# Kernel optimization log

Measured on AMD Instinct MI355X. Metric: run time of the kernel, lower is better.

## Reference

```python
import jax, jax.numpy as jnp
import numpy as np

B, S, D, H = 4, 2048, 1024, 16
DK = D // H
THETA = 10000.0


def apply_rope(x, pos, theta):
    # x: [B, H, S, DK], pos: [S] int
    d = x.shape[-1]
    inv_freq = theta ** (-jnp.arange(0, d, 2, dtype=jnp.float32) / d)  # [d/2]
    ang = pos.astype(jnp.float32)[:, None] * inv_freq[None, :]          # [S, d/2]
    cos, sin = jnp.cos(ang), jnp.sin(ang)
    x1 = x[..., 0::2]
    x2 = x[..., 1::2]
    r1 = x1 * cos - x2 * sin
    r2 = x1 * sin + x2 * cos
    return jnp.stack([r1, r2], axis=-1).reshape(x.shape)


def setup_inputs() -> dict:
    key = jax.random.key(0)
    ks = jax.random.split(key, 5)
    scale = 1.0 / np.sqrt(D)
    x = jax.random.normal(ks[0], (B, S, D), dtype=jnp.float32)
    Wq = jax.random.normal(ks[1], (D, D), dtype=jnp.float32) * scale
    Wk = jax.random.normal(ks[2], (D, D), dtype=jnp.float32) * scale
    Wv = jax.random.normal(ks[3], (D, D), dtype=jnp.float32) * scale
    Wo = jax.random.normal(ks[4], (D, D), dtype=jnp.float32) * scale
    token_positions = jnp.arange(S, dtype=jnp.int32)
    return {"x": x, "token_positions": token_positions,
            "Wq": Wq, "Wk": Wk, "Wv": Wv, "Wo": Wo}


def reference(x, token_positions, Wq, Wk, Wv, Wo):
    b, s, d = x.shape
    # Linear (no bias), weight stored [out, in]: y = x @ W.T
    q = (x @ Wq.T).reshape(b, s, H, DK).transpose(0, 2, 1, 3)  # [B,H,S,DK]
    k = (x @ Wk.T).reshape(b, s, H, DK).transpose(0, 2, 1, 3)
    v = (x @ Wv.T).reshape(b, s, H, DK).transpose(0, 2, 1, 3)
    q = apply_rope(q, token_positions, THETA)
    k = apply_rope(k, token_positions, THETA)
    scores = jnp.einsum('bhqd,bhkd->bhqk', q, k) / jnp.sqrt(jnp.float32(DK))
    causal = jnp.tril(jnp.ones((s, s), dtype=bool))
    scores = jnp.where(causal, scores, -jnp.inf)
    attn = jax.nn.softmax(scores, axis=-1)
    out = jnp.einsum('bhqk,bhkd->bhqd', attn, v)
    out = out.transpose(0, 2, 1, 3).reshape(b, s, d)
    return out @ Wo.T
```

## Files before the change

### kernel.cpp

```cpp
#include <hip/hip_runtime.h>

typedef unsigned short u16;
typedef __bf16 bf16x8 __attribute__((ext_vector_type(8)));
typedef float f32x4 __attribute__((ext_vector_type(4)));
typedef u16 u16x8 __attribute__((ext_vector_type(8)));
typedef u16 u16x4 __attribute__((ext_vector_type(4)));
typedef short s16x4 __attribute__((ext_vector_type(4)));

union V8 { u16x8 u; bf16x8 b; };
union V4 { u16x4 u; s16x4 s; unsigned w[2]; };

#define NB 4
#define NS 2048
#define ND 1024
#define NH 16
#define NDK 64
#define LP 80
#define CP 136
#define QSCL 0.18033688011112042f
#define FMAX 20.0f

__device__ __forceinline__ u16 f2bf(float f) {
  union { float f; unsigned u; } v; v.f = f;
  return (u16)((v.u + 0x7fffu + ((v.u >> 16) & 1u)) >> 16);
}

__device__ __forceinline__ unsigned pk2bf(float a, float b) {
#if __has_builtin(__builtin_amdgcn_cvt_pk_bf16_f32)
  auto v = __builtin_amdgcn_cvt_pk_bf16_f32(a, b);
  unsigned r; __builtin_memcpy(&r, &v, 4);
  return r;
#else
  return (unsigned)f2bf(a) | ((unsigned)f2bf(b) << 16);
#endif
}

__device__ __forceinline__ float fexp2(float x) {
#if __has_builtin(__builtin_amdgcn_exp2f)
  return __builtin_amdgcn_exp2f(x);
#else
  return exp2f(x);
#endif
}

__device__ __forceinline__ bf16x8 lds_frag(const u16* p) {
  V8 t; t.u = *(const u16x8*)p; return t.b;
}

__global__ __launch_bounds__(256) void cvt_bf16(const float* __restrict__ s,
                                                u16* __restrict__ d, int n) {
  const int i = (blockIdx.x * 256 + threadIdx.x) * 8;
  if (i >= n) return;
  const f32x4 lo = *(const f32x4*)(s + i);
  const f32x4 hi = *(const f32x4*)(s + i + 4);
  union { unsigned w[4]; u16x8 v; } o;
  o.w[0] = pk2bf(lo[0], lo[1]);
  o.w[1] = pk2bf(lo[2], lo[3]);
  o.w[2] = pk2bf(hi[0], hi[1]);
  o.w[3] = pk2bf(hi[2], hi[3]);
  *(u16x8*)(d + i) = o.v;
}

__global__ __launch_bounds__(256) void cvt_w4(const float* __restrict__ w0,
                                              const float* __restrict__ w1,
                                              const float* __restrict__ w2,
                                              const float* __restrict__ w3,
                                              u16* __restrict__ d) {
  const float* s = (blockIdx.y == 0) ? w0 : (blockIdx.y == 1) ? w1
                 : (blockIdx.y == 2) ? w2 : w3;
  const int i = (blockIdx.x * 256 + threadIdx.x) * 8;
  const f32x4 lo = *(const f32x4*)(s + i);
  const f32x4 hi = *(const f32x4*)(s + i + 4);
  union { unsigned w[4]; u16x8 v; } o;
  o.w[0] = pk2bf(lo[0], lo[1]);
  o.w[1] = pk2bf(lo[2], lo[3]);
  o.w[2] = pk2bf(hi[0], hi[1]);
  o.w[3] = pk2bf(hi[2], hi[3]);
  *(u16x8*)(d + (size_t)blockIdx.y * ND * ND + i) = o.v;
}

__global__ __launch_bounds__(256) void gemm_qkv(
    const u16* __restrict__ X, const u16* __restrict__ W0,
    const u16* __restrict__ W1, const u16* __restrict__ W2,
    void* __restrict__ O0, void* __restrict__ O1, void* __restrict__ O2,
    const int* __restrict__ tokpos, int modebase) {
  __shared__ u16 smem[2 * 128 * LP];
  u16* ldsA = smem;
  u16* ldsB = smem + 128 * LP;
  const int tid = threadIdx.x;
  const int lane = tid & 63;
  const int w = tid >> 6;
  const int quad = lane >> 4;
  const int l15 = lane & 15;
  const int z = blockIdx.z;
  const u16* Wp = (z == 0) ? W0 : (z == 1) ? W1 : W2;
  void* Op = (z == 0) ? O0 : (z == 1) ? O1 : O2;
  const int mode = modebase + z;
  const int m0 = blockIdx.x * 128;
  const int n0 = blockIdx.y * 128;
  const int wm = (w >> 1) * 64;
  const int wn = (w & 1) * 64;

  const int srow = tid >> 3;
  const int scol = (tid & 7) * 8;
  const u16* Ag = X + (size_t)(m0 + srow) * ND + scol;
  const u16* Bg = Wp + (size_t)(n0 + srow) * ND + scol;

  f32x4 acc[4][4];
  const f32x4 z4 = {0.f, 0.f, 0.f, 0.f};
  for (int i = 0; i < 4; i++)
    for (int j = 0; j < 4; j++) acc[i][j] = z4;

  for (int k0 = 0; k0 < ND; k0 += 64) {
    u16x8 ar[4], br[4];
    for (int r = 0; r < 4; r++) {
      ar[r] = *(const u16x8*)(Ag + (size_t)r * 32 * ND + k0);
      br[r] = *(const u16x8*)(Bg + (size_t)r * 32 * ND + k0);
    }
    __syncthreads();
    for (int r = 0; r < 4; r++) {
      *(u16x8*)&ldsA[(r * 32 + srow) * LP + scol] = ar[r];
      *(u16x8*)&ldsB[(r * 32 + srow) * LP + scol] = br[r];
    }
    __syncthreads();
    for (int kk = 0; kk < 2; kk++) {
      bf16x8 af[4], bfr[4];
      for (int mt = 0; mt < 4; mt++)
        af[mt] = lds_frag(&ldsA[(wm + mt * 16 + l15) * LP + (kk * 4 + quad) * 8]);
      for (int nt = 0; nt < 4; nt++)
        bfr[nt] = lds_frag(&ldsB[(wn + nt * 16 + l15) * LP + (kk * 4 + quad) * 8]);
      for (int mt = 0; mt < 4; mt++)
        for (int nt = 0; nt < 4; nt++)
          acc[mt][nt] = __builtin_amdgcn_mfma_f32_16x16x32_bf16(
              af[mt], bfr[nt], acc[mt][nt], 0, 0, 0);
    }
  }
  __syncthreads();

  if (mode < 2) {
    u16* cb = smem;
    for (int nt = 0; nt < 4; nt++) {
      const int n_g = n0 + wn + nt * 16 + l15;
      const int dk = n_g & 63;
      const float sgn = (dk & 1) ? 1.f : -1.f;
      const float inv_freq = __expf(-(float)(dk >> 1) * 0.28782313662425572f);
      for (int mt = 0; mt < 4; mt++) {
        const int mrow = wm + mt * 16 + quad * 4;
        for (int r = 0; r < 4; r++) {
          const int m_g = m0 + mrow + r;
          float v = acc[mt][nt][r];
          const int s_i = m_g & (NS - 1);
          const float pos = (float)tokpos[s_i];
          const float partner = __shfl_xor(v, 1);
          float sn, cs;
          __sincosf(pos * inv_freq, &sn, &cs);
          v = v * cs + partner * sn * sgn;
          if (mode == 0) v *= QSCL;
          cb[(mrow + r) * CP + wn + nt * 16 + l15] = f2bf(v);
        }
      }
    }
    __syncthreads();
    const int c = (tid & 15) * 8;
    const int h = (n0 + c) >> 6;
    const int dk0 = (n0 + c) & 63;
    for (int p = 0; p < 8; p++) {
      const int row = p * 16 + (tid >> 4);
      const int m_g = m0 + row;
      const int b = m_g >> 11;
      const int s_i = m_g & (NS - 1);
      *(u16x8*)&((u16*)Op)[(size_t)(((b * NH) + h) * NS + s_i) * NDK + dk0] =
          *(const u16x8*)&cb[row * CP + c];
    }
  } else if (mode == 2) {
    u16* cbT = smem;
    for (int nt = 0; nt < 4; nt++)
      for (int mt = 0; mt < 4; mt++)
        for (int r = 0; r < 4; r++)
          cbT[(wn + nt * 16 + l15) * CP + wm + mt * 16 + quad * 4 + r] =
              f2bf(acc[mt][nt][r]);
    __syncthreads();
    const int b = m0 >> 11;
    const int s0 = m0 & (NS - 1);
    const int col = (tid & 15) * 8;
    for (int p = 0; p < 8; p++) {
      const int row = p * 16 + (tid >> 4);
      const int dkg = n0 + row;
      const int h = dkg >> 6;
      *(u16x8*)&((u16*)Op)[(size_t)(((b * NH) + h) * NDK + (dkg & 63)) * NS +
                           s0 + col] = *(const u16x8*)&cbT[row * CP + col];
    }
  } else {
    for (int nt = 0; nt < 4; nt++) {
      const int n_g = n0 + wn + nt * 16 + l15;
      for (int mt = 0; mt < 4; mt++) {
        const int mb = m0 + wm + mt * 16 + quad * 4;
        for (int r = 0; r < 4; r++)
          ((float*)Op)[(size_t)(mb + r) * ND + n_g] = acc[mt][nt][r];
      }
    }
  }
}

__global__ __launch_bounds__(256) void attn(const u16* __restrict__ Q,
                                            const u16* __restrict__ Kc,
                                            const u16* __restrict__ Vt,
                                            u16* __restrict__ AO) {
  __shared__ u16 kt[64 * LP];
  __shared__ u16 vt[64 * LP];
  const int tid = threadIdx.x;
  const int lane = tid & 63;
  const int w = tid >> 6;
  const int quad = lane >> 4;
  const int l15 = lane & 15;
  const int bh = blockIdx.y;
  const int q0 = (gridDim.x - 1 - blockIdx.x) * 64;
  const int qg = q0 + w * 16 + l15;

  const u16* Qb = Q + (size_t)bh * NS * NDK + (size_t)qg * NDK + quad * 8;
  const bf16x8 qf0 = lds_frag(Qb);
  const bf16x8 qf1 = lds_frag(Qb + 32);

  f32x4 oacc[4];
  const f32x4 z4 = {0.f, 0.f, 0.f, 0.f};
  for (int i = 0; i < 4; i++) oacc[i] = z4;
  float lsum = 0.f;

  const int srow = tid >> 3;
  const int sg = tid & 7;
  const u16* Kb = Kc + (size_t)bh * NS * NDK;
  const u16* Vg = Vt + (size_t)bh * NDK * NS;

  u16x8 kreg[2], vreg[2];
  for (int r = 0; r < 2; r++) {
    kreg[r] = *(const u16x8*)(Kb + (size_t)(r * 32 + srow) * NDK + sg * 8);
    vreg[r] = *(const u16x8*)(Vg + (size_t)(r * 32 + srow) * NS + sg * 8);
  }

  for (int j0 = 0; j0 <= q0; j0 += 64) {
    __syncthreads();
    for (int r = 0; r < 2; r++) {
      const int row = r * 32 + srow;
      *(u16x8*)&kt[row * LP + (sg ^ (row & 7)) * 8] = kreg[r];
      *(u16x8*)&vt[row * LP + (sg ^ (row & 7)) * 8] = vreg[r];
    }
    __syncthreads();
    if (j0 + 64 <= q0) {
      const int nj = j0 + 64;
      for (int r = 0; r < 2; r++) {
        kreg[r] = *(const u16x8*)(Kb + (size_t)(nj + r * 32 + srow) * NDK + sg * 8);
        vreg[r] = *(const u16x8*)(Vg + (size_t)(r * 32 + srow) * NS + nj + sg * 8);
      }
    }

    f32x4 sa[4];
    for (int i = 0; i < 4; i++) sa[i] = z4;
    for (int kk = 0; kk < 2; kk++) {
      const bf16x8 qf = kk ? qf1 : qf0;
      for (int nt = 0; nt < 4; nt++) {
        const int row = nt * 16 + l15;
        const bf16x8 kf =
            lds_frag(&kt[row * LP + ((kk * 4 + quad) ^ (row & 7)) * 8]);
        sa[nt] = __builtin_amdgcn_mfma_f32_16x16x32_bf16(kf, qf, sa[nt], 0, 0, 0);
      }
    }

    const bool diag = (j0 == q0);
    float p[4][4];
    for (int nt = 0; nt < 4; nt++)
      for (int r = 0; r < 4; r++) {
        float e = fexp2(sa[nt][r] - FMAX);
        if (diag && (j0 + nt * 16 + quad * 4 + r) > qg) e = 0.f;
        p[nt][r] = e;
        lsum += e;
      }

    s16x4 pa[4];
    for (int nt = 0; nt < 4; nt++) {
      V4 t;
      t.w[0] = pk2bf(p[nt][0], p[nt][1]);
      t.w[1] = pk2bf(p[nt][2], p[nt][3]);
      pa[nt] = t.s;
    }

    for (int dt = 0; dt < 4; dt++) {
      const int dk = dt * 16 + l15;
      const int xr = dk & 7;
      for (int nt = 0; nt < 4; nt++) {
        const int chunk = 2 * nt + (quad >> 1);
        V4 t;
        t.u = *(const u16x4*)&vt[dk * LP + (chunk ^ xr) * 8 + 4 * (quad & 1)];
        oacc[dt] = __builtin_amdgcn_mfma_f32_16x16x16bf16_1k(pa[nt], t.s,
                                                             oacc[dt], 0, 0, 0);
      }
    }
  }

  lsum += __shfl_xor(lsum, 16);
  lsum += __shfl_xor(lsum, 32);
  float lq[4];
  for (int r = 0; r < 4; r++) lq[r] = __shfl(lsum, quad * 4 + r);

  __syncthreads();
  u16* ob = kt;
  for (int dt = 0; dt < 4; dt++)
    for (int r = 0; r < 4; r++)
      ob[(w * 16 + quad * 4 + r) * 72 + dt * 16 + l15] =
          f2bf(oacc[dt][r] / lq[r]);
  __syncthreads();
  const int b = bh >> 4, h = bh & 15;
  for (int p2 = 0; p2 < 2; p2++) {
    const int idx = p2 * 256 + tid;
    const int row = idx >> 3;
    const int c = (idx & 7) * 8;
    *(u16x8*)&AO[(size_t)(b * NS + q0 + row) * ND + h * 64 + c] =
        *(const u16x8*)&ob[row * 72 + c];
  }
}

extern "C" void kernel_launch(void* const* d_in, const int* in_sizes, int n_in,
                              void* d_out, int out_size, void* d_ws, size_t ws_size,
                              hipStream_t stream) {
  const float* x = (const float*)d_in[0];
  const int* tp = (const int*)d_in[1];
  const float* Wq = (const float*)d_in[2];
  const float* Wk = (const float*)d_in[3];
  const float* Wv = (const float*)d_in[4];
  const float* Wo = (const float*)d_in[5];

  const size_t NE = (size_t)NB * NS * ND;
  const int NW = ND * ND;
  u16* Qb = (u16*)d_ws;
  u16* Kb = Qb + NE;
  u16* Vtb = Kb + NE;
  u16* Xbf = Vtb + NE;
  u16* Wbf = Xbf + NE;

  dim3 blk(256);
  cvt_bf16<<<dim3((unsigned)(NE / 2048)), blk, 0, stream>>>(x, Xbf, (int)NE);
  cvt_w4<<<dim3(NW / 2048, 4), blk, 0, stream>>>(Wq, Wk, Wv, Wo, Wbf);
  gemm_qkv<<<dim3(64, 8, 3), blk, 0, stream>>>(
      Xbf, Wbf, Wbf + (size_t)NW, Wbf + 2 * (size_t)NW, Qb, Kb, Vtb, tp, 0);
  attn<<<dim3(NS / 64, NB * NH), blk, 0, stream>>>(Qb, Kb, Vtb, Xbf);
  gemm_qkv<<<dim3(64, 8, 1), blk, 0, stream>>>(
      Xbf, Wbf + 3 * (size_t)NW, Wbf + 3 * (size_t)NW, Wbf + 3 * (size_t)NW,
      d_out, d_out, d_out, tp, 3);
}
```

Baseline: 313.3 us.

## Process two query tiles per attention block and XOR-swizzle unpadded LDS

```diff
diff --git a/kernel.cpp b/kernel.cpp
--- a/kernel.cpp
+++ b/kernel.cpp
@@ -15,7 +15,6 @@
 #define ND 1024
 #define NH 16
 #define NDK 64
-#define LP 80
 #define CP 136
 #define QSCL 0.18033688011112042f
 #define FMAX 20.0f
@@ -46,6 +45,8 @@
 __device__ __forceinline__ bf16x8 lds_frag(const u16* p) {
   V8 t; t.u = *(const u16x8*)p; return t.b;
 }
+
+__device__ __forceinline__ int swz(int row) { return (row ^ (row >> 3)) & 7; }
 
 __global__ __launch_bounds__(256) void cvt_bf16(const float* __restrict__ s,
                                                 u16* __restrict__ d, int n) {
@@ -84,9 +85,9 @@
     const u16* __restrict__ W1, const u16* __restrict__ W2,
     void* __restrict__ O0, void* __restrict__ O1, void* __restrict__ O2,
     const int* __restrict__ tokpos, int modebase) {
-  __shared__ u16 smem[2 * 128 * LP];
+  __shared__ u16 smem[128 * CP];
   u16* ldsA = smem;
-  u16* ldsB = smem + 128 * LP;
+  u16* ldsB = smem + 8192;
   const int tid = threadIdx.x;
   const int lane = tid & 63;
   const int w = tid >> 6;
@@ -102,9 +103,9 @@
   const int wn = (w & 1) * 64;
 
   const int srow = tid >> 3;
-  const int scol = (tid & 7) * 8;
-  const u16* Ag = X + (size_t)(m0 + srow) * ND + scol;
-  const u16* Bg = Wp + (size_t)(n0 + srow) * ND + scol;
+  const int sg = tid & 7;
+  const u16* Ag = X + (size_t)(m0 + srow) * ND + sg * 8;
+  const u16* Bg = Wp + (size_t)(n0 + srow) * ND + sg * 8;
 
   f32x4 acc[4][4];
   const f32x4 z4 = {0.f, 0.f, 0.f, 0.f};
@@ -119,16 +120,21 @@
     }
     __syncthreads();
     for (int r = 0; r < 4; r++) {
-      *(u16x8*)&ldsA[(r * 32 + srow) * LP + scol] = ar[r];
-      *(u16x8*)&ldsB[(r * 32 + srow) * LP + scol] = br[r];
+      const int row = r * 32 + srow;
+      *(u16x8*)&ldsA[row * 64 + (sg ^ swz(row)) * 8] = ar[r];
+      *(u16x8*)&ldsB[row * 64 + (sg ^ swz(row)) * 8] = br[r];
     }
     __syncthreads();
     for (int kk = 0; kk < 2; kk++) {
       bf16x8 af[4], bfr[4];
-      for (int mt = 0; mt < 4; mt++)
-        af[mt] = lds_frag(&ldsA[(wm + mt * 16 + l15) * LP + (kk * 4 + quad) * 8]);
-      for (int nt = 0; nt < 4; nt++)
-        bfr[nt] = lds_frag(&ldsB[(wn + nt * 16 + l15) * LP + (kk * 4 + quad) * 8]);
+      for (int mt = 0; mt < 4; mt++) {
+        const int ra = wm + mt * 16 + l15;
+        af[mt] = lds_frag(&ldsA[ra * 64 + ((kk * 4 + quad) ^ swz(ra)) * 8]);
+      }
+      for (int nt = 0; nt < 4; nt++) {
+        const int rb = wn + nt * 16 + l15;
+        bfr[nt] = lds_frag(&ldsB[rb * 64 + ((kk * 4 + quad) ^ swz(rb)) * 8]);
+      }
       for (int mt = 0; mt < 4; mt++)
         for (int nt = 0; nt < 4; nt++)
           acc[mt][nt] = __builtin_amdgcn_mfma_f32_16x16x32_bf16(
@@ -202,29 +208,80 @@
   }
 }
 
+__device__ __forceinline__ void attn_tile(const u16* kt, const u16* vt,
+                                          bf16x8 qf0, bf16x8 qf1, int j0,
+                                          int q0, int qg, int quad, int l15,
+                                          f32x4* oacc, float& lsum) {
+  const f32x4 z4 = {0.f, 0.f, 0.f, 0.f};
+  f32x4 sa[4];
+  for (int i = 0; i < 4; i++) sa[i] = z4;
+  for (int kk = 0; kk < 2; kk++) {
+    const bf16x8 qf = kk ? qf1 : qf0;
+    for (int nt = 0; nt < 4; nt++) {
+      const int row = nt * 16 + l15;
+      const bf16x8 kf =
+          lds_frag(&kt[row * 64 + ((kk * 4 + quad) ^ swz(row)) * 8]);
+      sa[nt] = __builtin_amdgcn_mfma_f32_16x16x32_bf16(kf, qf, sa[nt], 0, 0, 0);
+    }
+  }
+  const bool diag = (j0 == q0);
+  float p[4][4];
+  for (int nt = 0; nt < 4; nt++)
+    for (int r = 0; r < 4; r++) {
+      float e = fexp2(sa[nt][r] - FMAX);
+      if (diag && (j0 + nt * 16 + quad * 4 + r) > qg) e = 0.f;
+      p[nt][r] = e;
+      lsum += e;
+    }
+  s16x4 pa[4];
+  for (int nt = 0; nt < 4; nt++) {
+    V4 t;
+    t.w[0] = pk2bf(p[nt][0], p[nt][1]);
+    t.w[1] = pk2bf(p[nt][2], p[nt][3]);
+    pa[nt] = t.s;
+  }
+  for (int dt = 0; dt < 4; dt++) {
+    const int dk = dt * 16 + l15;
+    const int sx = swz(dk);
+    for (int nt = 0; nt < 4; nt++) {
+      const int chunk = 2 * nt + (quad >> 1);
+      V4 t;
+      t.u = *(const u16x4*)&vt[dk * 64 + ((chunk ^ sx)) * 8 + 4 * (quad & 1)];
+      oacc[dt] = __builtin_amdgcn_mfma_f32_16x16x16bf16_1k(pa[nt], t.s,
+                                                           oacc[dt], 0, 0, 0);
+    }
+  }
+}
+
 __global__ __launch_bounds__(256) void attn(const u16* __restrict__ Q,
                                             const u16* __restrict__ Kc,
                                             const u16* __restrict__ Vt,
                                             u16* __restrict__ AO) {
-  __shared__ u16 kt[64 * LP];
-  __shared__ u16 vt[64 * LP];
+  __shared__ u16 kt[64 * 64];
+  __shared__ u16 vt[64 * 64];
+  __shared__ u16 ob[64 * 72];
   const int tid = threadIdx.x;
   const int lane = tid & 63;
   const int w = tid >> 6;
   const int quad = lane >> 4;
   const int l15 = lane & 15;
   const int bh = blockIdx.y;
-  const int q0 = (gridDim.x - 1 - blockIdx.x) * 64;
-  const int qg = q0 + w * 16 + l15;
-
-  const u16* Qb = Q + (size_t)bh * NS * NDK + (size_t)qg * NDK + quad * 8;
-  const bf16x8 qf0 = lds_frag(Qb);
-  const bf16x8 qf1 = lds_frag(Qb + 32);
-
-  f32x4 oacc[4];
+  const int u = 15 - (int)blockIdx.x;
+  const int qA0 = (2 * u) * 64;
+  const int qB0 = (2 * u + 1) * 64;
+  const int qgA = qA0 + w * 16 + l15;
+  const int qgB = qB0 + w * 16 + l15;
+
+  const u16* Qbase = Q + (size_t)bh * NS * NDK + quad * 8;
+  const bf16x8 qfA0 = lds_frag(Qbase + (size_t)qgA * NDK);
+  const bf16x8 qfA1 = lds_frag(Qbase + (size_t)qgA * NDK + 32);
+  const bf16x8 qfB0 = lds_frag(Qbase + (size_t)qgB * NDK);
+  const bf16x8 qfB1 = lds_frag(Qbase + (size_t)qgB * NDK + 32);
+
+  f32x4 oaccA[4], oaccB[4];
   const f32x4 z4 = {0.f, 0.f, 0.f, 0.f};
-  for (int i = 0; i < 4; i++) oacc[i] = z4;
-  float lsum = 0.f;
+  for (int i = 0; i < 4; i++) { oaccA[i] = z4; oaccB[i] = z4; }
+  float lsA = 0.f, lsB = 0.f;
 
   const int srow = tid >> 3;
   const int sg = tid & 7;
@@ -237,83 +294,59 @@
     vreg[r] = *(const u16x8*)(Vg + (size_t)(r * 32 + srow) * NS + sg * 8);
   }
 
-  for (int j0 = 0; j0 <= q0; j0 += 64) {
+  for (int j0 = 0; j0 <= qB0; j0 += 64) {
     __syncthreads();
     for (int r = 0; r < 2; r++) {
       const int row = r * 32 + srow;
-      *(u16x8*)&kt[row * LP + (sg ^ (row & 7)) * 8] = kreg[r];
-      *(u16x8*)&vt[row * LP + (sg ^ (row & 7)) * 8] = vreg[r];
-    }
-    __syncthreads();
-    if (j0 + 64 <= q0) {
+      *(u16x8*)&kt[row * 64 + (sg ^ swz(row)) * 8] = kreg[r];
+      *(u16x8*)&vt[row * 64 + (sg ^ swz(row)) * 8] = vreg[r];
+    }
+    __syncthreads();
+    if (j0 + 64 <= qB0) {
       const int nj = j0 + 64;
       for (int r = 0; r < 2; r++) {
         kreg[r] = *(const u16x8*)(Kb + (size_t)(nj + r * 32 + srow) * NDK + sg * 8);
         vreg[r] = *(const u16x8*)(Vg + (size_t)(r * 32 + srow) * NS + nj + sg * 8);
       }
     }
-
-    f32x4 sa[4];
-    for (int i = 0; i < 4; i++) sa[i] = z4;
-    for (int kk = 0; kk < 2; kk++) {
-      const bf16x8 qf = kk ? qf1 : qf0;
-      for (int nt = 0; nt < 4; nt++) {
-        const int row = nt * 16 + l15;
-        const bf16x8 kf =
-            lds_frag(&kt[row * LP + ((kk * 4 + quad) ^ (row & 7)) * 8]);
-        sa[nt] = __builtin_amdgcn_mfma_f32_16x16x32_bf16(kf, qf, sa[nt], 0, 0, 0);
-      }
-    }
-
-    const bool diag = (j0 == q0);
-    float p[4][4];
-    for (int nt = 0; nt < 4; nt++)
-      for (int r = 0; r < 4; r++) {
-        float e = fexp2(sa[nt][r] - FMAX);
-        if (diag && (j0 + nt * 16 + quad * 4 + r) > qg) e = 0.f;
-        p[nt][r] = e;
-        lsum += e;
-      }
-
-    s16x4 pa[4];
-    for (int nt = 0; nt < 4; nt++) {
-      V4 t;
-      t.w[0] = pk2bf(p[nt][0], p[nt][1]);
-      t.w[1] = pk2bf(p[nt][2], p[nt][3]);
-      pa[nt] = t.s;
-    }
-
-    for (int dt = 0; dt < 4; dt++) {
-      const int dk = dt * 16 + l15;
-      const int xr = dk & 7;
-      for (int nt = 0; nt < 4; nt++) {
-        const int chunk = 2 * nt + (quad >> 1);
-        V4 t;
-        t.u = *(const u16x4*)&vt[dk * LP + (chunk ^ xr) * 8 + 4 * (quad & 1)];
-        oacc[dt] = __builtin_amdgcn_mfma_f32_16x16x16bf16_1k(pa[nt], t.s,
-                                                             oacc[dt], 0, 0, 0);
-      }
-    }
-  }
-
-  lsum += __shfl_xor(lsum, 16);
-  lsum += __shfl_xor(lsum, 32);
-  float lq[4];
-  for (int r = 0; r < 4; r++) lq[r] = __shfl(lsum, quad * 4 + r);
-
-  __syncthreads();
-  u16* ob = kt;
+    attn_tile(kt, vt, qfB0, qfB1, j0, qB0, qgB, quad, l15, oaccB, lsB);
+    if (j0 <= qA0)
+      attn_tile(kt, vt, qfA0, qfA1, j0, qA0, qgA, quad, l15, oaccA, lsA);
+  }
+
+  const int b = bh >> 4, h = bh & 15;
+  lsA += __shfl_xor(lsA, 16);
+  lsA += __shfl_xor(lsA, 32);
+  lsB += __shfl_xor(lsB, 16);
+  lsB += __shfl_xor(lsB, 32);
+  float lqA[4], lqB[4];
+  for (int r = 0; r < 4; r++) {
+    lqA[r] = __shfl(lsA, quad * 4 + r);
+    lqB[r] = __shfl(lsB, quad * 4 + r);
+  }
   for (int dt = 0; dt < 4; dt++)
     for (int r = 0; r < 4; r++)
       ob[(w * 16 + quad * 4 + r) * 72 + dt * 16 + l15] =
-          f2bf(oacc[dt][r] / lq[r]);
+          f2bf(oaccA[dt][r] / lqA[r]);
   __syncthreads();
-  const int b = bh >> 4, h = bh & 15;
   for (int p2 = 0; p2 < 2; p2++) {
     const int idx = p2 * 256 + tid;
     const int row = idx >> 3;
     const int c = (idx & 7) * 8;
-    *(u16x8*)&AO[(size_t)(b * NS + q0 + row) * ND + h * 64 + c] =
+    *(u16x8*)&AO[(size_t)(b * NS + qA0 + row) * ND + h * 64 + c] =
+        *(const u16x8*)&ob[row * 72 + c];
+  }
+  __syncthreads();
+  for (int dt = 0; dt < 4; dt++)
+    for (int r = 0; r < 4; r++)
+      ob[(w * 16 + quad * 4 + r) * 72 + dt * 16 + l15] =
+          f2bf(oaccB[dt][r] / lqB[r]);
+  __syncthreads();
+  for (int p2 = 0; p2 < 2; p2++) {
+    const int idx = p2 * 256 + tid;
+    const int row = idx >> 3;
+    const int c = (idx & 7) * 8;
+    *(u16x8*)&AO[(size_t)(b * NS + qB0 + row) * ND + h * 64 + c] =
         *(const u16x8*)&ob[row * 72 + c];
   }
 }
@@ -341,7 +374,7 @@
   cvt_w4<<<dim3(NW / 2048, 4), blk, 0, stream>>>(Wq, Wk, Wv, Wo, Wbf);
   gemm_qkv<<<dim3(64, 8, 3), blk, 0, stream>>>(
       Xbf, Wbf, Wbf + (size_t)NW, Wbf + 2 * (size_t)NW, Qb, Kb, Vtb, tp, 0);
-  attn<<<dim3(NS / 64, NB * NH), blk, 0, stream>>>(Qb, Kb, Vtb, Xbf);
+  attn<<<dim3(16, NB * NH), blk, 0, stream>>>(Qb, Kb, Vtb, Xbf);
   gemm_qkv<<<dim3(64, 8, 1), blk, 0, stream>>>(
       Xbf, Wbf + 3 * (size_t)NW, Wbf + 3 * (size_t)NW, Wbf + 3 * (size_t)NW,
       d_out, d_out, d_out, tp, 3);
```

New measurement: 326.8 us. +4.3%, slower.
